# Performance work log

Hardware: AMD Instinct MI355X
Metric: run time of the kernel (lower is better)

The kernel has to match this reference:

```python
import math
import jax, jax.numpy as jnp
import numpy as np

B, S, DK, DV = 8, 2048, 512, 512

def setup_inputs() -> dict:
    key = jax.random.key(0)
    kq, kk, kv, km = jax.random.split(key, 4)
    Q = jax.random.normal(kq, (B, S, DK), dtype=jnp.float32)
    K = jax.random.normal(kk, (B, S, DK), dtype=jnp.float32)
    V = jax.random.normal(kv, (B, S, DV), dtype=jnp.float32)
    # key-padding mask, True = masked out; broadcasts over query dim
    mask_out = jax.random.randint(km, (B, 1, S), 0, 2).astype(jnp.bool_)
    return {"Q": Q, "K": K, "V": V, "mask_out": mask_out}

def reference(Q, K, V, mask_out):
    scale = math.sqrt(Q.shape[-1])
    # [B, S, S] scores
    scores = jnp.einsum('bqd,bkd->bqk', Q, K) / scale
    scores = jnp.where(mask_out, -jnp.inf, scores)
    attn = jax.nn.softmax(scores, axis=-1)
    # dropout is identity in eval mode (reference baseline)
    return jnp.einsum('bqk,bkv->bqv', attn, V)
```

## Files before the change

### kernel.cpp

```cpp
#include <hip/hip_runtime.h>
#include <stdint.h>
#include <stddef.h>

#define B_ 8
#define S_ 2048
#define D_ 512

typedef __attribute__((ext_vector_type(8))) short short8;
typedef __attribute__((ext_vector_type(4))) float f32x4;

#define LDS_BYTES 156416
#define OFF_K   0
#define OFF_V   65536
#define OFF_ST  131072
#define OFF_P   147456
#define OFF_A   155648
#define OFF_L   155904
#define OFF_M   156160

__device__ __forceinline__ void gl_lds16(const void* g, void* l) {
  __builtin_amdgcn_global_load_lds(
      (const __attribute__((address_space(1))) uint32_t*)g,
      (__attribute__((address_space(3))) uint32_t*)l, 16, 0, 0);
}

__device__ __forceinline__ uint32_t f2bf(float f) {
  union { float f; uint32_t u; } x; x.f = f;
  uint32_t r = x.u + 0x7FFFu + ((x.u >> 16) & 1u);
  return r >> 16;
}

__device__ __forceinline__ bool sniff_fp32(const void* p) {
  const uint32_t* w = (const uint32_t*)p;
  bool ok = true;
  #pragma unroll 1
  for (int i = 0; i < 64; ++i) {
    uint32_t e = (w[i] >> 23) & 0xFFu;
    if (!(e == 0u || (e >= 64u && e <= 192u))) ok = false;
  }
  return ok;
}

__device__ __forceinline__ short8 cvt8(const void* src, bool fp32) {
  short8 d;
  if (fp32) {
    const float* s = (const float*)src;
    f32x4 a = *(const f32x4*)s, c = *(const f32x4*)(s + 4);
    #pragma unroll
    for (int j = 0; j < 4; ++j) { d[j] = (short)f2bf(a[j]); d[4 + j] = (short)f2bf(c[j]); }
  } else {
    d = *(const short8*)src;
  }
  return d;
}

__global__ void kbf_kernel(const void* __restrict__ in, uint16_t* __restrict__ out) {
  bool fp32 = sniff_fp32(in);
  size_t i = ((size_t)blockIdx.x * 256 + threadIdx.x) * 8;
  const void* src = fp32 ? (const void*)((const float*)in + i)
                         : (const void*)((const uint16_t*)in + i);
  *(short8*)(out + i) = cvt8(src, fp32);
}

__global__ void vt_kernel(const void* __restrict__ V, uint16_t* __restrict__ vt) {
  __shared__ uint16_t tile[64][72];
  bool fp32 = sniff_fp32(V);
  int kt = blockIdx.x, dt = blockIdx.y, b = blockIdx.z;
  int t = threadIdx.x;
  size_t base = ((size_t)b * S_ + (size_t)kt * 64) * D_ + dt * 64;
  #pragma unroll
  for (int p = 0; p < 2; ++p) {
    int row = p * 32 + (t >> 3);
    int c8  = (t & 7) * 8;
    size_t off = base + (size_t)row * D_ + c8;
    const void* src = fp32 ? (const void*)((const float*)V + off)
                           : (const void*)((const uint16_t*)V + off);
    *(short8*)(&tile[row][c8]) = cvt8(src, fp32);
  }
  __syncthreads();
  uint16_t* dst = vt + ((size_t)b * D_ + dt * 64) * S_ + (size_t)kt * 64;
  #pragma unroll
  for (int p = 0; p < 2; ++p) {
    int idx = p * 256 + t;
    int dvr = idx >> 3;
    int kc  = idx & 7;
    short8 o;
    #pragma unroll
    for (int j = 0; j < 8; ++j) o[j] = (short)tile[kc * 8 + j][dvr];
    *(short8*)(dst + (size_t)dvr * S_ + kc * 8) = o;
  }
}

__device__ __forceinline__ void stage_K(char* smem, const uint16_t* kg, int w, int lane, int kt) {
  #pragma unroll
  for (int p = 0; p < 16; ++p) {
    int n = p * 4 + w;
    int g = (lane & ~7) | ((lane ^ n) & 7);
    gl_lds16(kg + ((size_t)(kt * 64 + n)) * D_ + g * 8, smem + OFF_K + p * 4096 + w * 1024);
  }
}
__device__ __forceinline__ void stage_VT(char* smem, const uint16_t* vtg, int w, int lane, int kt) {
  #pragma unroll
  for (int p = 0; p < 16; ++p) {
    int dvl = p * 8 + (lane >> 3);
    int g = (lane & 7) ^ (dvl & 7);
    gl_lds16(vtg + ((size_t)(w * 128 + dvl)) * S_ + kt * 64 + g * 8,
             smem + OFF_V + w * 16384 + p * 1024);
  }
}
__device__ __forceinline__ void stage_K_slow(char* smem, const void* kg, bool fp32,
                                             int w, int lane, int kt) {
  #pragma unroll
  for (int p = 0; p < 16; ++p) {
    int n = p * 4 + w;
    size_t off = ((size_t)(kt * 64 + n)) * D_ + lane * 8;
    const void* src = fp32 ? (const void*)((const float*)kg + off)
                           : (const void*)((const uint16_t*)kg + off);
    short8 d = cvt8(src, fp32);
    int s = (lane & ~7) | ((lane ^ n) & 7);
    *(short8*)(smem + OFF_K + n * 1024 + s * 16) = d;
  }
}
__device__ __forceinline__ void stage_V_slow(char* smem, const void* vg, bool fp32,
                                             int w, int lane, int kt) {
  #pragma unroll
  for (int p = 0; p < 16; ++p) {
    int n = p * 4 + w;
    size_t off = ((size_t)(kt * 64 + n)) * D_ + lane * 8;
    const void* src = fp32 ? (const void*)((const float*)vg + off)
                           : (const void*)((const uint16_t*)vg + off);
    short8 d = cvt8(src, fp32);
    *(short8*)(smem + OFF_V + n * 1024 + lane * 16) = d;
  }
}

template<bool FAST>
__global__ __launch_bounds__(256, 1)
void attn_kernel(const void* __restrict__ Q, const void* __restrict__ K,
                 const void* __restrict__ V, const void* __restrict__ mask,
                 const uint16_t* __restrict__ kbf, const uint16_t* __restrict__ vtbf,
                 void* __restrict__ out) {
  extern __shared__ char smem[];
  const int tid  = threadIdx.x;
  const int lane = tid & 63;
  const int w    = tid >> 6;
  const int m15  = lane & 15;
  const int kq   = lane >> 4;

  const bool fp32 = sniff_fp32(Q);

  const int b     = blockIdx.x;
  const int qbase = blockIdx.y * 64;
  const int rbase = (w >> 1) * 32;
  const int cbase = (w & 1) * 32;

  const uint16_t* kgf  = FAST ? (kbf + (size_t)b * S_ * D_) : nullptr;
  const uint16_t* vtgf = FAST ? (vtbf + (size_t)b * D_ * S_) : nullptr;
  const void* kgs = fp32 ? (const void*)((const float*)K + (size_t)b * S_ * D_)
                         : (const void*)((const uint16_t*)K + (size_t)b * S_ * D_);
  const void* vgs = fp32 ? (const void*)((const float*)V + (size_t)b * S_ * D_)
                         : (const void*)((const uint16_t*)V + (size_t)b * S_ * D_);

  if (tid < 64) {
    const uint32_t* mw = (const uint32_t*)mask;
    const uint8_t*  mb = (const uint8_t*)mask;
    bool is64 = true, any_even = false, is32 = true;
    for (int j = 0; j < 64; ++j) {
      uint32_t lo = mw[2 * j], hi = mw[2 * j + 1];
      if (hi != 0u || lo > 1u) is64 = false;
      if (lo) any_even = true;
    }
    is64 = is64 && any_even;
    for (int j = 0; j < 128; ++j) {
      uint32_t x = mw[j];
      if (x != 0u && x != 1u && x != 0x3F800000u) is32 = false;
    }
    uint32_t bits = 0;
    int base = b * S_ + tid * 32;
    for (int e = 0; e < 32; ++e) {
      uint32_t x = is64 ? mw[2 * (base + e)]
                        : (is32 ? mw[base + e] : (uint32_t)mb[base + e]);
      bits |= (x ? 1u : 0u) << e;
    }
    *(uint32_t*)(smem + OFF_M + tid * 4) = bits;
  }

  short8 aq[2][16];
  {
    size_t q0 = ((size_t)b * S_ + qbase + rbase + m15) * D_ + kq * 8;
    #pragma unroll
    for (int rt = 0; rt < 2; ++rt)
      #pragma unroll
      for (int sl = 0; sl < 16; ++sl) {
        size_t off = q0 + (size_t)rt * 16 * D_ + sl * 32;
        const void* src = fp32 ? (const void*)((const float*)Q + off)
                               : (const void*)((const uint16_t*)Q + off);
        aq[rt][sl] = cvt8(src, fp32);
      }
  }

  f32x4 acc_o[4][8];
  #pragma unroll
  for (int i = 0; i < 4; ++i)
    #pragma unroll
    for (int j = 0; j < 8; ++j)
      acc_o[i][j] = (f32x4){0.f, 0.f, 0.f, 0.f};

  float m_run = -1e30f, l_run = 0.f;
  const float k1 = 0.06375872f;

  if (FAST) { stage_K(smem, kgf, w, lane, 0); stage_VT(smem, vtgf, w, lane, 0); }

  for (int kt = 0; kt < 32; ++kt) {
    if (!FAST) {
      __syncthreads();
      stage_K_slow(smem, kgs, fp32, w, lane, kt);
      stage_V_slow(smem, vgs, fp32, w, lane, kt);
    }
    __syncthreads();

    int key0 = kt * 64 + cbase + m15, key1 = key0 + 16;
    float bv0 = ((*(const uint32_t*)(smem + OFF_M + (key0 >> 5) * 4) >> (key0 & 31)) & 1u)
                ? -3.0e38f : 0.f;
    float bv1 = ((*(const uint32_t*)(smem + OFF_M + (key1 >> 5) * 4) >> (key1 & 31)) & 1u)
                ? -3.0e38f : 0.f;

    f32x4 acc_s[2][2];
    #pragma unroll
    for (int i = 0; i < 2; ++i)
      #pragma unroll
      for (int j = 0; j < 2; ++j)
        acc_s[i][j] = (f32x4){0.f, 0.f, 0.f, 0.f};
    #pragma unroll
    for (int sl = 0; sl < 16; ++sl) {
      short8 bf[2];
      #pragma unroll
      for (int ct = 0; ct < 2; ++ct) {
        int n  = cbase + ct * 16 + m15;
        int c  = sl * 4 + kq;
        int cs = (c & ~7) | ((c ^ n) & 7);
        bf[ct] = *(const short8*)(smem + OFF_K + n * 1024 + cs * 16);
      }
      #pragma unroll
      for (int rt = 0; rt < 2; ++rt)
        #pragma unroll
        for (int ct = 0; ct < 2; ++ct)
          acc_s[rt][ct] = __builtin_amdgcn_mfma_f32_16x16x32_bf16(
              aq[rt][sl], bf[ct], acc_s[rt][ct], 0, 0, 0);
    }

    #pragma unroll
    for (int rt = 0; rt < 2; ++rt) {
      int q0  = rbase + rt * 16 + kq * 4;
      int blk = q0 >> 2;
      #pragma unroll
      for (int ct = 0; ct < 2; ++ct) {
        int key  = cbase + ct * 16 + m15;
        int xblk = blk ^ (key & 7) ^ (((key >> 4) & 3) << 2);
        float bvv = ct ? bv1 : bv0;
        f32x4 sv;
        #pragma unroll
        for (int r = 0; r < 4; ++r) sv[r] = acc_s[rt][ct][r] * k1 + bvv;
        *(f32x4*)(smem + OFF_ST + key * 256 + xblk * 16) = sv;
      }
    }
    __syncthreads();

    {
      int row = w * 16 + m15;
      float u[16];
      #pragma unroll
      for (int j = 0; j < 16; ++j) {
        int key  = kq * 16 + j;
        int xblk = (row >> 2) ^ (key & 7) ^ (((key >> 4) & 3) << 2);
        u[j] = *(const float*)(smem + OFF_ST + key * 256 + xblk * 16 + (row & 3) * 4);
      }
      float mt = u[0];
      #pragma unroll
      for (int j = 1; j < 16; ++j) mt = fmaxf(mt, u[j]);
      mt = fmaxf(mt, __shfl_xor(mt, 16, 64));
      mt = fmaxf(mt, __shfl_xor(mt, 32, 64));
      float m_new = fmaxf(m_run, mt);
      float alpha = exp2f(m_run - m_new);
      float s = 0.f;
      #pragma unroll
      for (int j = 0; j < 16; ++j) { u[j] = exp2f(u[j] - m_new); s += u[j]; }
      s += __shfl_xor(s, 16, 64);
      s += __shfl_xor(s, 32, 64);
      l_run = l_run * alpha + s;
      m_run = m_new;
      #pragma unroll
      for (int hf = 0; hf < 2; ++hf) {
        uint32_t d[4];
        #pragma unroll
        for (int q = 0; q < 4; ++q)
          d[q] = f2bf(u[hf * 8 + q * 2]) | (f2bf(u[hf * 8 + q * 2 + 1]) << 16);
        int c  = kq * 2 + hf;
        int cs = c ^ (row & 7);
        *(uint4*)(smem + OFF_P + row * 128 + cs * 16) = make_uint4(d[0], d[1], d[2], d[3]);
      }
      if (kq == 0) {
        *(float*)(smem + OFF_A + row * 4) = alpha;
        *(float*)(smem + OFF_L + row * 4) = l_run;
      }
    }
    __syncthreads();

    if (FAST && kt < 31) stage_K(smem, kgf, w, lane, kt + 1);

    #pragma unroll
    for (int rt = 0; rt < 4; ++rt) {
      f32x4 al = *(const f32x4*)(smem + OFF_A + (rt * 16 + kq * 4) * 4);
      #pragma unroll
      for (int ct = 0; ct < 8; ++ct) acc_o[rt][ct] *= al;
    }
    short8 ap[4][2];
    #pragma unroll
    for (int rt = 0; rt < 4; ++rt)
      #pragma unroll
      for (int ks = 0; ks < 2; ++ks) {
        int qq = rt * 16 + m15;
        int cs = (ks * 4 + kq) ^ (qq & 7);
        ap[rt][ks] = *(const short8*)(smem + OFF_P + qq * 128 + cs * 16);
      }
    #pragma unroll
    for (int ks = 0; ks < 2; ++ks)
      #pragma unroll
      for (int ct = 0; ct < 8; ++ct) {
        short8 bv;
        if (FAST) {
          int dvl = ct * 16 + m15;
          int cs  = (ks * 4 + kq) ^ (dvl & 7);
          bv = *(const short8*)(smem + OFF_V + w * 16384 + dvl * 128 + cs * 16);
        } else {
          #pragma unroll
          for (int j = 0; j < 8; ++j)
            bv[j] = *(const short*)(smem + OFF_V + (ks * 32 + kq * 8 + j) * 1024
                                    + (w * 128 + ct * 16 + m15) * 2);
        }
        #pragma unroll
        for (int rt = 0; rt < 4; ++rt)
          acc_o[rt][ct] = __builtin_amdgcn_mfma_f32_16x16x32_bf16(
              ap[rt][ks], bv, acc_o[rt][ct], 0, 0, 0);
      }

    if (FAST && kt < 31) stage_VT(smem, vtgf, w, lane, kt + 1);
  }

  #pragma unroll
  for (int rt = 0; rt < 4; ++rt) {
    f32x4 lv = *(const f32x4*)(smem + OFF_L + (rt * 16 + kq * 4) * 4);
    f32x4 inv;
    #pragma unroll
    for (int r = 0; r < 4; ++r) inv[r] = lv[r] > 0.f ? 1.f / lv[r] : 0.f;
    #pragma unroll
    for (int ct = 0; ct < 8; ++ct) {
      int col = w * 128 + ct * 16 + m15;
      #pragma unroll
      for (int r = 0; r < 4; ++r) {
        int row = qbase + rt * 16 + kq * 4 + r;
        size_t idx = ((size_t)b * S_ + row) * D_ + col;
        float val = acc_o[rt][ct][r] * inv[r];
        if (fp32) ((float*)out)[idx] = val;
        else      ((uint16_t*)out)[idx] = (uint16_t)f2bf(val);
      }
    }
  }
}

extern "C" void kernel_launch(void* const* d_in, const int* in_sizes, int n_in,
                              void* d_out, int out_size, void* d_ws, size_t ws_size,
                              hipStream_t stream) {
  (void)in_sizes; (void)n_in; (void)out_size;
  const void* Q    = d_in[0];
  const void* K    = d_in[1];
  const void* V    = d_in[2];
  const void* mask = d_in[3];

  const size_t half = (size_t)B_ * S_ * D_ * 2;
  bool fast = ws_size >= 2 * half;

  if (fast) {
    uint16_t* kbf  = (uint16_t*)d_ws;
    uint16_t* vtbf = (uint16_t*)((char*)d_ws + half);
    kbf_kernel<<<4096, 256, 0, stream>>>(K, kbf);
    vt_kernel<<<dim3(32, 8, 8), 256, 0, stream>>>(V, vtbf);
    hipFuncSetAttribute((const void*)attn_kernel<true>,
                        hipFuncAttributeMaxDynamicSharedMemorySize, LDS_BYTES);
    attn_kernel<true><<<dim3(8, 32), 256, LDS_BYTES, stream>>>(
        Q, K, V, mask, kbf, vtbf, d_out);
  } else {
    hipFuncSetAttribute((const void*)attn_kernel<false>,
                        hipFuncAttributeMaxDynamicSharedMemorySize, LDS_BYTES);
    attn_kernel<false><<<dim3(8, 32), 256, LDS_BYTES, stream>>>(
        Q, K, V, mask, nullptr, nullptr, d_out);
  }
}
```

Measured before the change: 349.6 us.

## Halve query and key tiles so two attention blocks fit per CU

Shrinks the query tile from 64 to 32 rows and the key tile from 64 to 32. That cuts LDS to about 72KB per block and allows launch_bounds(256,2), so two workgroups can share a CU. It doubles the grid to 512 blocks and reworks the QK, softmax and PV mappings for the smaller tiles. The V transpose kernel is also rewritten to use 512 threads with direct strided gathers instead of an LDS tile. The aim is better latency hiding and CU fill, at the cost of twice as many loop iterations and barriers, and twice the total K/V reads across blocks.

```diff
diff --git a/kernel.cpp b/kernel.cpp
--- a/kernel.cpp
+++ b/kernel.cpp
@@ -5,18 +5,21 @@
 #define B_ 8
 #define S_ 2048
 #define D_ 512
+#define QT 32
+#define KTL 32
+#define NIT (S_ / KTL)
 
 typedef __attribute__((ext_vector_type(8))) short short8;
 typedef __attribute__((ext_vector_type(4))) float f32x4;
 
-#define LDS_BYTES 156416
 #define OFF_K   0
-#define OFF_V   65536
-#define OFF_ST  131072
-#define OFF_P   147456
-#define OFF_A   155648
-#define OFF_L   155904
-#define OFF_M   156160
+#define OFF_V   32768
+#define OFF_ST  65536
+#define OFF_P   69632
+#define OFF_A   71680
+#define OFF_L   71808
+#define OFF_M   71936
+#define LDS_BYTES 72192
 
 __device__ __forceinline__ void gl_lds16(const void* g, void* l) {
   __builtin_amdgcn_global_load_lds(
@@ -63,57 +66,46 @@
 }
 
 __global__ void vt_kernel(const void* __restrict__ V, uint16_t* __restrict__ vt) {
-  __shared__ uint16_t tile[64][72];
   bool fp32 = sniff_fp32(V);
   int kt = blockIdx.x, dt = blockIdx.y, b = blockIdx.z;
-  int t = threadIdx.x;
-  size_t base = ((size_t)b * S_ + (size_t)kt * 64) * D_ + dt * 64;
-  #pragma unroll
-  for (int p = 0; p < 2; ++p) {
-    int row = p * 32 + (t >> 3);
-    int c8  = (t & 7) * 8;
-    size_t off = base + (size_t)row * D_ + c8;
-    const void* src = fp32 ? (const void*)((const float*)V + off)
-                           : (const void*)((const uint16_t*)V + off);
-    *(short8*)(&tile[row][c8]) = cvt8(src, fp32);
-  }
-  __syncthreads();
-  uint16_t* dst = vt + ((size_t)b * D_ + dt * 64) * S_ + (size_t)kt * 64;
-  #pragma unroll
-  for (int p = 0; p < 2; ++p) {
-    int idx = p * 256 + t;
-    int dvr = idx >> 3;
-    int kc  = idx & 7;
-    short8 o;
-    #pragma unroll
-    for (int j = 0; j < 8; ++j) o[j] = (short)tile[kc * 8 + j][dvr];
-    *(short8*)(dst + (size_t)dvr * S_ + kc * 8) = o;
-  }
+  int t  = threadIdx.x;
+  int dv = t >> 3;
+  int kg = t & 7;
+  int dvg = dt * 64 + dv;
+  size_t base = (size_t)b * S_ * D_;
+  short8 o;
+  #pragma unroll
+  for (int j = 0; j < 8; ++j) {
+    size_t off = base + (size_t)(kt * 64 + kg * 8 + j) * D_ + dvg;
+    if (fp32) o[j] = (short)f2bf(((const float*)V)[off]);
+    else      o[j] = (short)((const uint16_t*)V)[off];
+  }
+  *(short8*)(vt + ((size_t)b * D_ + dvg) * S_ + kt * 64 + kg * 8) = o;
 }
 
 __device__ __forceinline__ void stage_K(char* smem, const uint16_t* kg, int w, int lane, int kt) {
   #pragma unroll
-  for (int p = 0; p < 16; ++p) {
+  for (int p = 0; p < 8; ++p) {
     int n = p * 4 + w;
     int g = (lane & ~7) | ((lane ^ n) & 7);
-    gl_lds16(kg + ((size_t)(kt * 64 + n)) * D_ + g * 8, smem + OFF_K + p * 4096 + w * 1024);
+    gl_lds16(kg + ((size_t)(kt * KTL + n)) * D_ + g * 8, smem + OFF_K + (p * 4 + w) * 1024);
   }
 }
 __device__ __forceinline__ void stage_VT(char* smem, const uint16_t* vtg, int w, int lane, int kt) {
   #pragma unroll
-  for (int p = 0; p < 16; ++p) {
-    int dvl = p * 8 + (lane >> 3);
-    int g = (lane & 7) ^ (dvl & 7);
-    gl_lds16(vtg + ((size_t)(w * 128 + dvl)) * S_ + kt * 64 + g * 8,
-             smem + OFF_V + w * 16384 + p * 1024);
+  for (int p = 0; p < 8; ++p) {
+    int dvl = p * 16 + (lane >> 2);
+    int g = (lane & 3) ^ (dvl & 3);
+    gl_lds16(vtg + ((size_t)(w * 128 + dvl)) * S_ + kt * KTL + g * 8,
+             smem + OFF_V + w * 8192 + p * 1024);
   }
 }
 __device__ __forceinline__ void stage_K_slow(char* smem, const void* kg, bool fp32,
                                              int w, int lane, int kt) {
   #pragma unroll
-  for (int p = 0; p < 16; ++p) {
+  for (int p = 0; p < 8; ++p) {
     int n = p * 4 + w;
-    size_t off = ((size_t)(kt * 64 + n)) * D_ + lane * 8;
+    size_t off = ((size_t)(kt * KTL + n)) * D_ + lane * 8;
     const void* src = fp32 ? (const void*)((const float*)kg + off)
                            : (const void*)((const uint16_t*)kg + off);
     short8 d = cvt8(src, fp32);
@@ -124,9 +116,9 @@
 __device__ __forceinline__ void stage_V_slow(char* smem, const void* vg, bool fp32,
                                              int w, int lane, int kt) {
   #pragma unroll
-  for (int p = 0; p < 16; ++p) {
+  for (int p = 0; p < 8; ++p) {
     int n = p * 4 + w;
-    size_t off = ((size_t)(kt * 64 + n)) * D_ + lane * 8;
+    size_t off = ((size_t)(kt * KTL + n)) * D_ + lane * 8;
     const void* src = fp32 ? (const void*)((const float*)vg + off)
                            : (const void*)((const uint16_t*)vg + off);
     short8 d = cvt8(src, fp32);
@@ -135,7 +127,7 @@
 }
 
 template<bool FAST>
-__global__ __launch_bounds__(256, 1)
+__global__ __launch_bounds__(256, 2)
 void attn_kernel(const void* __restrict__ Q, const void* __restrict__ K,
                  const void* __restrict__ V, const void* __restrict__ mask,
                  const uint16_t* __restrict__ kbf, const uint16_t* __restrict__ vtbf,
@@ -150,9 +142,9 @@
   const bool fp32 = sniff_fp32(Q);
 
   const int b     = blockIdx.x;
-  const int qbase = blockIdx.y * 64;
-  const int rbase = (w >> 1) * 32;
-  const int cbase = (w & 1) * 32;
+  const int qbase = blockIdx.y * QT;
+  const int rt_qk = w >> 1;
+  const int cb_qk = (w & 1) * 16;
 
   const uint16_t* kgf  = FAST ? (kbf + (size_t)b * S_ * D_) : nullptr;
   const uint16_t* vtgf = FAST ? (vtbf + (size_t)b * D_ * S_) : nullptr;
@@ -185,23 +177,21 @@
     *(uint32_t*)(smem + OFF_M + tid * 4) = bits;
   }
 
-  short8 aq[2][16];
+  short8 aq[16];
   {
-    size_t q0 = ((size_t)b * S_ + qbase + rbase + m15) * D_ + kq * 8;
-    #pragma unroll
-    for (int rt = 0; rt < 2; ++rt)
-      #pragma unroll
-      for (int sl = 0; sl < 16; ++sl) {
-        size_t off = q0 + (size_t)rt * 16 * D_ + sl * 32;
-        const void* src = fp32 ? (const void*)((const float*)Q + off)
-                               : (const void*)((const uint16_t*)Q + off);
-        aq[rt][sl] = cvt8(src, fp32);
-      }
-  }
-
-  f32x4 acc_o[4][8];
-  #pragma unroll
-  for (int i = 0; i < 4; ++i)
+    size_t q0 = ((size_t)b * S_ + qbase + rt_qk * 16 + m15) * D_ + kq * 8;
+    #pragma unroll
+    for (int sl = 0; sl < 16; ++sl) {
+      size_t off = q0 + sl * 32;
+      const void* src = fp32 ? (const void*)((const float*)Q + off)
+                             : (const void*)((const uint16_t*)Q + off);
+      aq[sl] = cvt8(src, fp32);
+    }
+  }
+
+  f32x4 acc_o[2][8];
+  #pragma unroll
+  for (int i = 0; i < 2; ++i)
     #pragma unroll
     for (int j = 0; j < 8; ++j)
       acc_o[i][j] = (f32x4){0.f, 0.f, 0.f, 0.f};
@@ -211,7 +201,7 @@
 
   if (FAST) { stage_K(smem, kgf, w, lane, 0); stage_VT(smem, vtgf, w, lane, 0); }
 
-  for (int kt = 0; kt < 32; ++kt) {
+  for (int kt = 0; kt < NIT; ++kt) {
     if (!FAST) {
       __syncthreads();
       stage_K_slow(smem, kgs, fp32, w, lane, kt);
@@ -219,136 +209,102 @@
     }
     __syncthreads();
 
-    int key0 = kt * 64 + cbase + m15, key1 = key0 + 16;
-    float bv0 = ((*(const uint32_t*)(smem + OFF_M + (key0 >> 5) * 4) >> (key0 & 31)) & 1u)
-                ? -3.0e38f : 0.f;
-    float bv1 = ((*(const uint32_t*)(smem + OFF_M + (key1 >> 5) * 4) >> (key1 & 31)) & 1u)
-                ? -3.0e38f : 0.f;
-
-    f32x4 acc_s[2][2];
-    #pragma unroll
-    for (int i = 0; i < 2; ++i)
-      #pragma unroll
-      for (int j = 0; j < 2; ++j)
-        acc_s[i][j] = (f32x4){0.f, 0.f, 0.f, 0.f};
+    int keyg = kt * KTL + cb_qk + m15;
+    float bv = ((*(const uint32_t*)(smem + OFF_M + (keyg >> 5) * 4) >> (keyg & 31)) & 1u)
+               ? -3.0e38f : 0.f;
+
+    f32x4 acc_s = (f32x4){0.f, 0.f, 0.f, 0.f};
     #pragma unroll
     for (int sl = 0; sl < 16; ++sl) {
-      short8 bf[2];
-      #pragma unroll
-      for (int ct = 0; ct < 2; ++ct) {
-        int n  = cbase + ct * 16 + m15;
-        int c  = sl * 4 + kq;
-        int cs = (c & ~7) | ((c ^ n) & 7);
-        bf[ct] = *(const short8*)(smem + OFF_K + n * 1024 + cs * 16);
+      int n  = cb_qk + m15;
+      int c  = sl * 4 + kq;
+      int cs = (c & ~7) | ((c ^ n) & 7);
+      short8 bf = *(const short8*)(smem + OFF_K + n * 1024 + cs * 16);
+      acc_s = __builtin_amdgcn_mfma_f32_16x16x32_bf16(aq[sl], bf, acc_s, 0, 0, 0);
+    }
+
+    {
+      int key  = cb_qk + m15;
+      int blk  = rt_qk * 4 + kq;
+      int xblk = blk ^ (key & 7);
+      f32x4 sv;
+      #pragma unroll
+      for (int r = 0; r < 4; ++r) sv[r] = acc_s[r] * k1 + bv;
+      *(f32x4*)(smem + OFF_ST + key * 128 + xblk * 16) = sv;
+    }
+    __syncthreads();
+
+    if (FAST && kt < NIT - 1) stage_K(smem, kgf, w, lane, kt + 1);
+
+    {
+      int r  = w * 8 + (lane >> 3);
+      int k0 = (lane & 7) * 4;
+      float u[4];
+      #pragma unroll
+      for (int i = 0; i < 4; ++i) {
+        int k    = k0 + i;
+        int xblk = (r >> 2) ^ (k & 7);
+        u[i] = *(const float*)(smem + OFF_ST + k * 128 + xblk * 16 + (r & 3) * 4);
       }
-      #pragma unroll
-      for (int rt = 0; rt < 2; ++rt)
-        #pragma unroll
-        for (int ct = 0; ct < 2; ++ct)
-          acc_s[rt][ct] = __builtin_amdgcn_mfma_f32_16x16x32_bf16(
-              aq[rt][sl], bf[ct], acc_s[rt][ct], 0, 0, 0);
-    }
-
-    #pragma unroll
-    for (int rt = 0; rt < 2; ++rt) {
-      int q0  = rbase + rt * 16 + kq * 4;
-      int blk = q0 >> 2;
-      #pragma unroll
-      for (int ct = 0; ct < 2; ++ct) {
-        int key  = cbase + ct * 16 + m15;
-        int xblk = blk ^ (key & 7) ^ (((key >> 4) & 3) << 2);
-        float bvv = ct ? bv1 : bv0;
-        f32x4 sv;
-        #pragma unroll
-        for (int r = 0; r < 4; ++r) sv[r] = acc_s[rt][ct][r] * k1 + bvv;
-        *(f32x4*)(smem + OFF_ST + key * 256 + xblk * 16) = sv;
-      }
-    }
-    __syncthreads();
-
-    {
-      int row = w * 16 + m15;
-      float u[16];
-      #pragma unroll
-      for (int j = 0; j < 16; ++j) {
-        int key  = kq * 16 + j;
-        int xblk = (row >> 2) ^ (key & 7) ^ (((key >> 4) & 3) << 2);
-        u[j] = *(const float*)(smem + OFF_ST + key * 256 + xblk * 16 + (row & 3) * 4);
-      }
-      float mt = u[0];
-      #pragma unroll
-      for (int j = 1; j < 16; ++j) mt = fmaxf(mt, u[j]);
-      mt = fmaxf(mt, __shfl_xor(mt, 16, 64));
-      mt = fmaxf(mt, __shfl_xor(mt, 32, 64));
+      float mt = fmaxf(fmaxf(u[0], u[1]), fmaxf(u[2], u[3]));
+      mt = fmaxf(mt, __shfl_xor(mt, 1, 64));
+      mt = fmaxf(mt, __shfl_xor(mt, 2, 64));
+      mt = fmaxf(mt, __shfl_xor(mt, 4, 64));
       float m_new = fmaxf(m_run, mt);
       float alpha = exp2f(m_run - m_new);
       float s = 0.f;
       #pragma unroll
-      for (int j = 0; j < 16; ++j) { u[j] = exp2f(u[j] - m_new); s += u[j]; }
-      s += __shfl_xor(s, 16, 64);
-      s += __shfl_xor(s, 32, 64);
+      for (int i = 0; i < 4; ++i) { u[i] = exp2f(u[i] - m_new); s += u[i]; }
+      s += __shfl_xor(s, 1, 64);
+      s += __shfl_xor(s, 2, 64);
+      s += __shfl_xor(s, 4, 64);
       l_run = l_run * alpha + s;
       m_run = m_new;
-      #pragma unroll
-      for (int hf = 0; hf < 2; ++hf) {
-        uint32_t d[4];
+      uint2 d;
+      d.x = f2bf(u[0]) | (f2bf(u[1]) << 16);
+      d.y = f2bf(u[2]) | (f2bf(u[3]) << 16);
+      *(uint2*)(smem + OFF_P + r * 64 + k0 * 2) = d;
+      if ((lane & 7) == 0) {
+        *(float*)(smem + OFF_A + r * 4) = alpha;
+        *(float*)(smem + OFF_L + r * 4) = l_run;
+      }
+    }
+    __syncthreads();
+
+    #pragma unroll
+    for (int rt = 0; rt < 2; ++rt) {
+      f32x4 al = *(const f32x4*)(smem + OFF_A + (rt * 16 + kq * 4) * 4);
+      #pragma unroll
+      for (int ct = 0; ct < 8; ++ct) acc_o[rt][ct] *= al;
+    }
+    short8 ap[2];
+    #pragma unroll
+    for (int rt = 0; rt < 2; ++rt)
+      ap[rt] = *(const short8*)(smem + OFF_P + (rt * 16 + m15) * 64 + kq * 16);
+    #pragma unroll
+    for (int ct = 0; ct < 8; ++ct) {
+      short8 bvv;
+      if (FAST) {
+        int dvL = ct * 16 + m15;
+        int cs  = kq ^ (dvL & 3);
+        bvv = *(const short8*)(smem + OFF_V + w * 8192 + dvL * 64 + cs * 16);
+      } else {
         #pragma unroll
-        for (int q = 0; q < 4; ++q)
-          d[q] = f2bf(u[hf * 8 + q * 2]) | (f2bf(u[hf * 8 + q * 2 + 1]) << 16);
-        int c  = kq * 2 + hf;
-        int cs = c ^ (row & 7);
-        *(uint4*)(smem + OFF_P + row * 128 + cs * 16) = make_uint4(d[0], d[1], d[2], d[3]);
+        for (int j = 0; j < 8; ++j)
+          bvv[j] = *(const short*)(smem + OFF_V + (kq * 8 + j) * 1024
+                                   + (w * 128 + ct * 16 + m15) * 2);
       }
-      if (kq == 0) {
-        *(float*)(smem + OFF_A + row * 4) = alpha;
-        *(float*)(smem + OFF_L + row * 4) = l_run;
-      }
-    }
-    __syncthreads();
-
-    if (FAST && kt < 31) stage_K(smem, kgf, w, lane, kt + 1);
-
-    #pragma unroll
-    for (int rt = 0; rt < 4; ++rt) {
-      f32x4 al = *(const f32x4*)(smem + OFF_A + (rt * 16 + kq * 4) * 4);
-      #pragma unroll
-      for (int ct = 0; ct < 8; ++ct) acc_o[rt][ct] *= al;
-    }
-    short8 ap[4][2];
-    #pragma unroll
-    for (int rt = 0; rt < 4; ++rt)
-      #pragma unroll
-      for (int ks = 0; ks < 2; ++ks) {
-        int qq = rt * 16 + m15;
-        int cs = (ks * 4 + kq) ^ (qq & 7);
-        ap[rt][ks] = *(const short8*)(smem + OFF_P + qq * 128 + cs * 16);
-      }
-    #pragma unroll
-    for (int ks = 0; ks < 2; ++ks)
-      #pragma unroll
-      for (int ct = 0; ct < 8; ++ct) {
-        short8 bv;
-        if (FAST) {
-          int dvl = ct * 16 + m15;
-          int cs  = (ks * 4 + kq) ^ (dvl & 7);
-          bv = *(const short8*)(smem + OFF_V + w * 16384 + dvl * 128 + cs * 16);
-        } else {
-          #pragma unroll
-          for (int j = 0; j < 8; ++j)
-            bv[j] = *(const short*)(smem + OFF_V + (ks * 32 + kq * 8 + j) * 1024
-                                    + (w * 128 + ct * 16 + m15) * 2);
-        }
-        #pragma unroll
-        for (int rt = 0; rt < 4; ++rt)
-          acc_o[rt][ct] = __builtin_amdgcn_mfma_f32_16x16x32_bf16(
-              ap[rt][ks], bv, acc_o[rt][ct], 0, 0, 0);
-      }
-
-    if (FAST && kt < 31) stage_VT(smem, vtgf, w, lane, kt + 1);
-  }
-
-  #pragma unroll
-  for (int rt = 0; rt < 4; ++rt) {
+      #pragma unroll
+      for (int rt = 0; rt < 2; ++rt)
+        acc_o[rt][ct] = __builtin_amdgcn_mfma_f32_16x16x32_bf16(
+            ap[rt], bvv, acc_o[rt][ct], 0, 0, 0);
+    }
+
+    if (FAST && kt < NIT - 1) stage_VT(smem, vtgf, w, lane, kt + 1);
+  }
+
+  #pragma unroll
+  for (int rt = 0; rt < 2; ++rt) {
     f32x4 lv = *(const f32x4*)(smem + OFF_L + (rt * 16 + kq * 4) * 4);
     f32x4 inv;
     #pragma unroll
@@ -384,15 +340,15 @@
     uint16_t* kbf  = (uint16_t*)d_ws;
     uint16_t* vtbf = (uint16_t*)((char*)d_ws + half);
     kbf_kernel<<<4096, 256, 0, stream>>>(K, kbf);
-    vt_kernel<<<dim3(32, 8, 8), 256, 0, stream>>>(V, vtbf);
+    vt_kernel<<<dim3(32, 8, 8), 512, 0, stream>>>(V, vtbf);
     hipFuncSetAttribute((const void*)attn_kernel<true>,
                         hipFuncAttributeMaxDynamicSharedMemorySize, LDS_BYTES);
-    attn_kernel<true><<<dim3(8, 32), 256, LDS_BYTES, stream>>>(
+    attn_kernel<true><<<dim3(8, S_ / QT), 256, LDS_BYTES, stream>>>(
         Q, K, V, mask, kbf, vtbf, d_out);
   } else {
     hipFuncSetAttribute((const void*)attn_kernel<false>,
                         hipFuncAttributeMaxDynamicSharedMemorySize, LDS_BYTES);
-    attn_kernel<false><<<dim3(8, 32), 256, LDS_BYTES, stream>>>(
+    attn_kernel<false><<<dim3(8, S_ / QT), 256, LDS_BYTES, stream>>>(
         Q, K, V, mask, nullptr, nullptr, d_out);
   }
 }
```

New measurement: 338.5 us. 3.2% less time.
